# Kernel tuning notes

Measured on AMD Instinct MI355X. Metric: run time of the kernel, lower is better.

## Reference

```python
import jax, jax.numpy as jnp
import numpy as np

B, N, C, H = 8, 4096, 512, 8
HD = C // H  # head_dim = 64
SCALE = HD ** -0.5


def setup_inputs() -> dict:
    key = jax.random.key(0)
    k1, k2, k3, k4 = jax.random.split(key, 4)
    x1 = jax.random.normal(k1, (B, N, C), dtype=jnp.float32)
    x2 = jax.random.normal(k2, (B, N, C), dtype=jnp.float32)
    # nn.Linear(dim, 2*dim, bias=False) weights; stored as [in, out] for x @ W
    lim = 1.0 / np.sqrt(C)
    W_kv1 = jax.random.uniform(k3, (C, 2 * C), dtype=jnp.float32, minval=-lim, maxval=lim)
    W_kv2 = jax.random.uniform(k4, (C, 2 * C), dtype=jnp.float32, minval=-lim, maxval=lim)
    return {"x1": x1, "x2": x2, "W_kv1": W_kv1, "W_kv2": W_kv2}


def _heads(t):
    # [B, N, C] -> [B, H, N, HD]
    return t.reshape(B, N, H, HD).transpose(0, 2, 1, 3)


def _kv(x, W):
    kv = (x @ W).reshape(B, N, 2, H, HD)  # [B, N, 2, H, HD]
    kv = kv.transpose(2, 0, 3, 1, 4)      # [2, B, H, N, HD]
    return kv[0], kv[1]


def _ctx(k, v):
    # K^T V: [B, H, HD, HD], scaled then softmax over axis -2 (the k-feature axis)
    ctx = jnp.einsum("bhnd,bhne->bhde", k, v) * SCALE
    return jax.nn.softmax(ctx, axis=-2)


def reference(x1, x2, W_kv1, W_kv2):
    q1 = _heads(x1)
    q2 = _heads(x2)
    k1, v1 = _kv(x1, W_kv1)
    k2, v2 = _kv(x2, W_kv2)
    ctx1 = _ctx(k1, v1)
    ctx2 = _ctx(k2, v2)
    # cross: q1 attends via ctx2, q2 via ctx1
    o1 = jnp.einsum("bhnd,bhde->bhne", q1, ctx2).transpose(0, 2, 1, 3).reshape(B, N, C)
    o2 = jnp.einsum("bhnd,bhde->bhne", q2, ctx1).transpose(0, 2, 1, 3).reshape(B, N, C)
    return o1, o2
```

## Files before the change

### kernel.cpp

```cpp
#include <hip/hip_runtime.h>
#include <stdint.h>
#include <stddef.h>

#define NB 8
#define NSEQ 4096
#define NC 512
#define NH 8
#define SWZ(c) ((((c) >> 2) ^ (c)) & 7)

typedef __attribute__((ext_vector_type(4))) float f4;
typedef __attribute__((ext_vector_type(8))) short bf8;
typedef __attribute__((ext_vector_type(4))) short bf4;
typedef __attribute__((ext_vector_type(2))) unsigned int u32x2;
typedef __attribute__((ext_vector_type(4))) unsigned int u32x4;

__device__ __forceinline__ short f2bf(float f) {
  union { float f; unsigned int u; } v; v.f = f;
  unsigned int u = v.u + 0x7FFFu + ((v.u >> 16) & 1u);
  return (short)(u >> 16);
}
__device__ __forceinline__ float bf2f(short h) {
  union { unsigned int u; float f; } v;
  v.u = ((unsigned int)(unsigned short)h) << 16;
  return v.f;
}
__device__ __forceinline__ unsigned int cvtpk(float a, float b) {
  unsigned int r;
  asm("v_cvt_pk_bf16_f32 %0, %1, %2" : "=v"(r) : "v"(a), "v"(b));
  return r;
}

__global__ __launch_bounds__(256) void k_wt(const float* __restrict__ W0,
                                            const float* __restrict__ W1,
                                            short* __restrict__ Wth,
                                            short* __restrict__ Wtl) {
  __shared__ float t[64 * 65];
  int bid = blockIdx.x;
  int ot = bid & 15;
  int ct = (bid >> 4) & 7;
  int s = bid >> 7;
  const float* W = s ? W1 : W0;
  const float* src = W + (size_t)(ct * 64) * 1024 + ot * 64;
  int tid = threadIdx.x;
  int rr = tid >> 4, c4 = (tid & 15) * 4;
#pragma unroll
  for (int p = 0; p < 4; ++p) {
    int c = p * 16 + rr;
    f4 v = *(const f4*)&src[(size_t)c * 1024 + c4];
#pragma unroll
    for (int i = 0; i < 4; ++i) t[(c4 + i) * 65 + c] = v[i];
  }
  __syncthreads();
  size_t obase = (size_t)s * 524288 + (size_t)(ot * 64) * 512 + ct * 64;
#pragma unroll
  for (int p = 0; p < 4; ++p) {
    int o = p * 16 + rr;
    bf4 vh, vl;
#pragma unroll
    for (int i = 0; i < 4; ++i) {
      float v = t[o * 65 + c4 + i];
      short h = f2bf(v);
      vh[i] = h; vl[i] = f2bf(v - bf2f(h));
    }
    *(bf4*)&Wth[obase + (size_t)o * 512 + c4] = vh;
    *(bf4*)&Wtl[obase + (size_t)o * 512 + c4] = vl;
  }
}

__global__ __launch_bounds__(256, 3) void k_gram(const float* __restrict__ x0,
                                                 const float* __restrict__ x1,
                                                 float* __restrict__ G32a,
                                                 float* __restrict__ G32b) {
  __shared__ short bfA[64 * 128];
  __shared__ short bfB[64 * 128];
  int bid = blockIdx.x;
  int xcd = bid & 7;
  int j = bid >> 3;
  int kh = j >= 72;
  int jj = j - kh * 72;
  int sb = xcd + ((jj >= 36) ? 8 : 0);
  int p = (jj >= 36) ? (jj - 36) : jj;
  int ti = 0;
  while (p >= 8 - ti) { p -= 8 - ti; ++ti; }
  int tj = ti + p;
  int diag = (ti == tj);
  int s = sb >> 3, b = sb & 7;
  const float* x = s ? x1 : x0;
  const float* Axp = x + (size_t)b * NSEQ * NC + (size_t)kh * 2048 * NC + ti * 64;
  const float* Bxp = x + (size_t)b * NSEQ * NC + (size_t)kh * 2048 * NC + tj * 64;
  int tid = threadIdx.x;
  int lane = tid & 63;
  int w = tid >> 6;
  int c4 = (tid & 15) * 4;
  int n4 = (tid >> 4) * 4;
  int wr = w & 1, wc = w >> 1;
  int mrow = lane & 15;
  int kreg = lane >> 4;
  f4 z = {0.f, 0.f, 0.f, 0.f};
  f4 acc[2][2];
#pragma unroll
  for (int i = 0; i < 2; ++i)
#pragma unroll
    for (int jq = 0; jq < 2; ++jq) acc[i][jq] = z;

  f4 va[8], vb[8];
  auto load = [&](int k0) {
#pragma unroll
    for (int gq = 0; gq < 2; ++gq)
#pragma unroll
      for (int i = 0; i < 4; ++i)
        va[gq * 4 + i] = *(const f4*)&Axp[(size_t)(k0 + gq * 64 + n4 + i) * NC + c4];
    if (!diag) {
#pragma unroll
      for (int gq = 0; gq < 2; ++gq)
#pragma unroll
        for (int i = 0; i < 4; ++i)
          vb[gq * 4 + i] = *(const f4*)&Bxp[(size_t)(k0 + gq * 64 + n4 + i) * NC + c4];
    }
  };
  auto store = [&]() {
#pragma unroll
    for (int gq = 0; gq < 2; ++gq)
#pragma unroll
      for (int ci = 0; ci < 4; ++ci) {
        int c = c4 + ci;
        int slot = gq * 8 + (((n4 >> 3) ^ SWZ(c)) & 7);
        int soff = c * 128 + slot * 8 + (n4 & 7);
        u32x2 wa;
        wa[0] = cvtpk(va[gq * 4 + 0][ci], va[gq * 4 + 1][ci]);
        wa[1] = cvtpk(va[gq * 4 + 2][ci], va[gq * 4 + 3][ci]);
        *(u32x2*)&bfA[soff] = wa;
        if (!diag) {
          u32x2 wb;
          wb[0] = cvtpk(vb[gq * 4 + 0][ci], vb[gq * 4 + 1][ci]);
          wb[1] = cvtpk(vb[gq * 4 + 2][ci], vb[gq * 4 + 3][ci]);
          *(u32x2*)&bfB[soff] = wb;
        }
      }
  };
  auto comp = [&]() {
    const short* Bbuf = diag ? bfA : bfB;
#pragma unroll
    for (int kk = 0; kk < 4; ++kk) {
      int gr = kk * 4 + kreg;
      bf8 a[2], bb[2];
#pragma unroll
      for (int i = 0; i < 2; ++i) {
        int ra = wr * 32 + i * 16 + mrow;
        int sa = (gr & 8) | ((gr ^ SWZ(ra)) & 7);
        a[i] = *(const bf8*)&bfA[ra * 128 + sa * 8];
        int rb2 = wc * 32 + i * 16 + mrow;
        int sb2 = (gr & 8) | ((gr ^ SWZ(rb2)) & 7);
        bb[i] = *(const bf8*)&Bbuf[rb2 * 128 + sb2 * 8];
      }
#pragma unroll
      for (int i = 0; i < 2; ++i)
#pragma unroll
        for (int jq = 0; jq < 2; ++jq)
          acc[i][jq] = __builtin_amdgcn_mfma_f32_16x16x32_bf16(a[i], bb[jq], acc[i][jq], 0, 0, 0);
    }
  };

  load(0);
  for (int it = 0; it < 16; ++it) {
    store();
    __syncthreads();
    if (it < 15) load((it + 1) * 128);
    __builtin_amdgcn_sched_barrier(0);
    comp();
    __syncthreads();
  }

  float* Gp = (kh ? G32b : G32a) + (size_t)sb * NC * NC;
  int rb = ti * 64 + wr * 32 + (lane >> 4) * 4;
  int cb = tj * 64 + wc * 32 + (lane & 15);
#pragma unroll
  for (int i = 0; i < 2; ++i)
#pragma unroll
    for (int jq = 0; jq < 2; ++jq)
#pragma unroll
      for (int r = 0; r < 4; ++r)
        Gp[(size_t)(rb + i * 16 + r) * NC + cb + jq * 16] = acc[i][jq][r];
}

__global__ __launch_bounds__(256) void k_sym(const float* __restrict__ G32a,
                                             const float* __restrict__ G32b,
                                             short* __restrict__ Gh,
                                             short* __restrict__ Gl) {
  __shared__ float t[64 * 65];
  int bid = blockIdx.x;
  int tile = bid & 63;
  int sb = bid >> 6;
  int ti = tile >> 3, tj = tile & 7;
  int tr = ti > tj;
  size_t soff = (size_t)sb * 262144
              + (tr ? ((size_t)(tj * 64) * 512 + ti * 64)
                    : ((size_t)(ti * 64) * 512 + tj * 64));
  const float* srcA = G32a + soff;
  const float* srcB = G32b + soff;
  int tid = threadIdx.x;
  int rr = tid >> 4;
  int c4 = (tid & 15) * 4;
#pragma unroll
  for (int p = 0; p < 4; ++p) {
    int r = p * 16 + rr;
    f4 v = *(const f4*)&srcA[(size_t)r * 512 + c4];
    f4 v2 = *(const f4*)&srcB[(size_t)r * 512 + c4];
    v += v2;
    if (tr) {
#pragma unroll
      for (int i = 0; i < 4; ++i) t[(c4 + i) * 65 + r] = v[i];
    } else {
#pragma unroll
      for (int i = 0; i < 4; ++i) t[r * 65 + c4 + i] = v[i];
    }
  }
  __syncthreads();
  size_t obase = (size_t)sb * 262144 + (size_t)(ti * 64) * 512 + tj * 64;
#pragma unroll
  for (int p = 0; p < 4; ++p) {
    int r = p * 16 + rr;
    bf4 vh, vl;
#pragma unroll
    for (int i = 0; i < 4; ++i) {
      float v = t[r * 65 + c4 + i] * 0.125f;
      short h = f2bf(v);
      vh[i] = h; vl[i] = f2bf(v - bf2f(h));
    }
    *(bf4*)&Gh[obase + (size_t)r * 512 + c4] = vh;
    *(bf4*)&Gl[obase + (size_t)r * 512 + c4] = vl;
  }
}

__global__ __launch_bounds__(256) void k_t(const short* __restrict__ Wth,
                                           const short* __restrict__ Wtl,
                                           const short* __restrict__ Gh,
                                           const short* __restrict__ Gl,
                                           float* __restrict__ Ttf) {
  __shared__ short Ah[128 * 40];
  __shared__ short Al[128 * 40];
  __shared__ short Bh[128 * 40];
  __shared__ short Bl[128 * 40];
  int tid = threadIdx.x;
  int et = blockIdx.x & 3;
  int ct = blockIdx.x >> 2;
  int sb = blockIdx.y;
  int s = sb >> 3;
  const short* Avh = Wth + ((size_t)s * 1024 + 512 + (size_t)et * 128) * NC;
  const short* Avl = Wtl + ((size_t)s * 1024 + 512 + (size_t)et * 128) * NC;
  const short* Gph = Gh + (size_t)sb * 262144 + (size_t)(ct * 128) * 512;
  const short* Gpl = Gl + (size_t)sb * 262144 + (size_t)(ct * 128) * 512;
  int cc = tid >> 1;
  int kh = (tid & 1) * 16;
  int lane = tid & 63;
  int w = tid >> 6;
  int wm = (w & 1) * 64;
  int wn = (w >> 1) * 64;
  int mrow = lane & 15;
  int kcol = (lane >> 4) * 8;
  f4 z = {0.f, 0.f, 0.f, 0.f};
  f4 acc[4][4];
#pragma unroll
  for (int i = 0; i < 4; ++i)
#pragma unroll
    for (int j = 0; j < 4; ++j) acc[i][j] = z;

  for (int it = 0; it < 16; ++it) {
    int k0 = it * 32;
    __syncthreads();
    *(bf8*)&Ah[cc * 40 + kh]     = *(const bf8*)&Avh[(size_t)cc * NC + k0 + kh];
    *(bf8*)&Ah[cc * 40 + kh + 8] = *(const bf8*)&Avh[(size_t)cc * NC + k0 + kh + 8];
    *(bf8*)&Al[cc * 40 + kh]     = *(const bf8*)&Avl[(size_t)cc * NC + k0 + kh];
    *(bf8*)&Al[cc * 40 + kh + 8] = *(const bf8*)&Avl[(size_t)cc * NC + k0 + kh + 8];
    *(bf8*)&Bh[cc * 40 + kh]     = *(const bf8*)&Gph[(size_t)cc * 512 + k0 + kh];
    *(bf8*)&Bh[cc * 40 + kh + 8] = *(const bf8*)&Gph[(size_t)cc * 512 + k0 + kh + 8];
    *(bf8*)&Bl[cc * 40 + kh]     = *(const bf8*)&Gpl[(size_t)cc * 512 + k0 + kh];
    *(bf8*)&Bl[cc * 40 + kh + 8] = *(const bf8*)&Gpl[(size_t)cc * 512 + k0 + kh + 8];
    __syncthreads();
    bf8 ah[4], al[4], bh[4], bl[4];
#pragma unroll
    for (int i = 0; i < 4; ++i) {
      ah[i] = *(const bf8*)&Ah[(wm + i * 16 + mrow) * 40 + kcol];
      al[i] = *(const bf8*)&Al[(wm + i * 16 + mrow) * 40 + kcol];
      bh[i] = *(const bf8*)&Bh[(wn + i * 16 + mrow) * 40 + kcol];
      bl[i] = *(const bf8*)&Bl[(wn + i * 16 + mrow) * 40 + kcol];
    }
#pragma unroll
    for (int i = 0; i < 4; ++i)
#pragma unroll
      for (int j = 0; j < 4; ++j) {
        acc[i][j] = __builtin_amdgcn_mfma_f32_16x16x32_bf16(ah[i], bh[j], acc[i][j], 0, 0, 0);
        acc[i][j] = __builtin_amdgcn_mfma_f32_16x16x32_bf16(ah[i], bl[j], acc[i][j], 0, 0, 0);
        acc[i][j] = __builtin_amdgcn_mfma_f32_16x16x32_bf16(al[i], bh[j], acc[i][j], 0, 0, 0);
      }
  }
  float* Tp = Ttf + (size_t)sb * NC * NC;
  int rb = et * 128 + wm + (lane >> 4) * 4;
  int cb = ct * 128 + wn + (lane & 15);
#pragma unroll
  for (int i = 0; i < 4; ++i)
#pragma unroll
    for (int j = 0; j < 4; ++j)
#pragma unroll
      for (int r = 0; r < 4; ++r)
        Tp[(size_t)(rb + i * 16 + r) * NC + cb + j * 16] = acc[i][j][r];
}

__global__ __launch_bounds__(256) void k_ctx(const short* __restrict__ Wth,
                                             const short* __restrict__ Wtl,
                                             const float* __restrict__ Ttf,
                                             short* __restrict__ ctxT) {
  __shared__ short Ah[64 * 72];
  __shared__ short Al[64 * 72];
  __shared__ short Bh[64 * 72];
  __shared__ short Bl[64 * 72];
  __shared__ float Sf[64 * 68];
  int tid = threadIdx.x;
  int h = blockIdx.x & 7;
  int sb = blockIdx.x >> 3;
  int s = sb >> 3;
  const short* Akh = Wth + ((size_t)s * 1024 + (size_t)h * 64) * NC;
  const short* Akl = Wtl + ((size_t)s * 1024 + (size_t)h * 64) * NC;
  const float* Bt = Ttf + ((size_t)sb * NC + (size_t)h * 64) * NC;
  int cs = tid >> 3;
  int kg = (tid & 7) * 8;
  int lane = tid & 63;
  int w = tid >> 6;
  int mrow = lane & 15;
  int kcol = (lane >> 4) * 8;
  f4 z = {0.f, 0.f, 0.f, 0.f};
  f4 acc[4];
#pragma unroll
  for (int j = 0; j < 4; ++j) acc[j] = z;

  for (int it = 0; it < 8; ++it) {
    int k0 = it * 64;
    __syncthreads();
#pragma unroll
    for (int r = 0; r < 2; ++r) {
      int d = cs + r * 32;
      *(bf8*)&Ah[d * 72 + kg] = *(const bf8*)&Akh[(size_t)d * NC + k0 + kg];
      *(bf8*)&Al[d * 72 + kg] = *(const bf8*)&Akl[(size_t)d * NC + k0 + kg];
      f4 g0 = *(const f4*)&Bt[(size_t)d * NC + k0 + kg];
      f4 g1 = *(const f4*)&Bt[(size_t)d * NC + k0 + kg + 4];
      bf8 vh, vl;
#pragma unroll
      for (int i = 0; i < 4; ++i) {
        short hh = f2bf(g0[i]);
        vh[i] = hh; vl[i] = f2bf(g0[i] - bf2f(hh));
        hh = f2bf(g1[i]);
        vh[i + 4] = hh; vl[i + 4] = f2bf(g1[i] - bf2f(hh));
      }
      *(bf8*)&Bh[d * 72 + kg] = vh;
      *(bf8*)&Bl[d * 72 + kg] = vl;
    }
    __syncthreads();
#pragma unroll
    for (int kk = 0; kk < 2; ++kk) {
      bf8 ah = *(const bf8*)&Ah[(w * 16 + mrow) * 72 + kk * 32 + kcol];
      bf8 al = *(const bf8*)&Al[(w * 16 + mrow) * 72 + kk * 32 + kcol];
#pragma unroll
      for (int j = 0; j < 4; ++j) {
        bf8 bh = *(const bf8*)&Bh[(j * 16 + mrow) * 72 + kk * 32 + kcol];
        bf8 bl = *(const bf8*)&Bl[(j * 16 + mrow) * 72 + kk * 32 + kcol];
        acc[j] = __builtin_amdgcn_mfma_f32_16x16x32_bf16(ah, bh, acc[j], 0, 0, 0);
        acc[j] = __builtin_amdgcn_mfma_f32_16x16x32_bf16(ah, bl, acc[j], 0, 0, 0);
        acc[j] = __builtin_amdgcn_mfma_f32_16x16x32_bf16(al, bh, acc[j], 0, 0, 0);
      }
    }
  }
  __syncthreads();
#pragma unroll
  for (int j = 0; j < 4; ++j)
#pragma unroll
    for (int r = 0; r < 4; ++r)
      Sf[(w * 16 + (lane >> 4) * 4 + r) * 68 + j * 16 + (lane & 15)] = acc[j][r];
  __syncthreads();
  if (tid < 64) {
    int e = tid;
    float mx = -1e30f;
    for (int d = 0; d < 64; ++d) mx = fmaxf(mx, Sf[d * 68 + e]);
    float sum = 0.f;
    for (int d = 0; d < 64; ++d) {
      float ev = __expf(Sf[d * 68 + e] - mx);
      sum += ev;
      Sf[d * 68 + e] = ev;
    }
    float rs = 1.f / sum;
    short* cp = ctxT + (((size_t)sb * NH + h) * 64 + e) * 64;
    for (int d0 = 0; d0 < 64; d0 += 4) {
      bf4 ov;
      ov[0] = f2bf(Sf[(d0 + 0) * 68 + e] * rs);
      ov[1] = f2bf(Sf[(d0 + 1) * 68 + e] * rs);
      ov[2] = f2bf(Sf[(d0 + 2) * 68 + e] * rs);
      ov[3] = f2bf(Sf[(d0 + 3) * 68 + e] * rs);
      *(bf4*)&cp[d0] = ov;
    }
  }
}

__global__ __launch_bounds__(256) void k_o(const float* __restrict__ x0,
                                           const float* __restrict__ x1,
                                           const short* __restrict__ ctxT,
                                           float* __restrict__ out) {
  __shared__ short Ab[128 * 72];
  __shared__ short Bb[64 * 72];
  int tid = threadIdx.x;
  int bx = blockIdx.x;
  int nt = bx & 31;
  int h = (bx >> 5) & 7;
  int b = (bx >> 8) & 7;
  int so = bx >> 11;
  const float* x = so ? x1 : x0;
  const short* cp = ctxT + (((size_t)(1 - so) * NB + b) * NH + h) * 64 * 64;
  {
    int e = tid >> 2;
    int dg = (tid & 3) * 16;
    *(bf8*)&Bb[e * 72 + dg] = *(const bf8*)&cp[e * 64 + dg];
    *(bf8*)&Bb[e * 72 + dg + 8] = *(const bf8*)&cp[e * 64 + dg + 8];
  }
  const float* xp = x + ((size_t)b * NSEQ + (size_t)nt * 128) * NC + h * 64;
  {
    int n = tid >> 1;
    int dh = (tid & 1) * 32;
    const float* row = xp + (size_t)n * NC + dh;
#pragma unroll
    for (int q = 0; q < 4; ++q) {
      f4 v0 = *(const f4*)&row[q * 8];
      f4 v1 = *(const f4*)&row[q * 8 + 4];
      u32x4 pw;
      pw[0] = cvtpk(v0[0], v0[1]);
      pw[1] = cvtpk(v0[2], v0[3]);
      pw[2] = cvtpk(v1[0], v1[1]);
      pw[3] = cvtpk(v1[2], v1[3]);
      *(u32x4*)&Ab[n * 72 + dh + q * 8] = pw;
    }
  }
  __syncthreads();
  int lane = tid & 63;
  int w = tid >> 6;
  int mrow = lane & 15;
  int kcol = (lane >> 4) * 8;
  f4 z = {0.f, 0.f, 0.f, 0.f};
  f4 acc[2][4];
#pragma unroll
  for (int i = 0; i < 2; ++i)
#pragma unroll
    for (int j = 0; j < 4; ++j) acc[i][j] = z;
#pragma unroll
  for (int kk = 0; kk < 2; ++kk) {
    bf8 a0 = *(const bf8*)&Ab[(w * 32 + mrow) * 72 + kk * 32 + kcol];
    bf8 a1 = *(const bf8*)&Ab[(w * 32 + 16 + mrow) * 72 + kk * 32 + kcol];
#pragma unroll
    for (int j = 0; j < 4; ++j) {
      bf8 bv = *(const bf8*)&Bb[(j * 16 + mrow) * 72 + kk * 32 + kcol];
      acc[0][j] = __builtin_amdgcn_mfma_f32_16x16x32_bf16(a0, bv, acc[0][j], 0, 0, 0);
      acc[1][j] = __builtin_amdgcn_mfma_f32_16x16x32_bf16(a1, bv, acc[1][j], 0, 0, 0);
    }
  }
  float* op = out + (size_t)so * ((size_t)NB * NSEQ * NC)
            + ((size_t)b * NSEQ + (size_t)nt * 128) * NC + h * 64;
#pragma unroll
  for (int i = 0; i < 2; ++i)
#pragma unroll
    for (int j = 0; j < 4; ++j)
#pragma unroll
      for (int r = 0; r < 4; ++r)
        op[(size_t)(w * 32 + i * 16 + (lane >> 4) * 4 + r) * NC + j * 16 + (lane & 15)] = acc[i][j][r];
}

extern "C" void kernel_launch(void* const* d_in, const int* in_sizes, int n_in,
                              void* d_out, int out_size, void* d_ws, size_t ws_size,
                              hipStream_t stream) {
  const float* x1 = (const float*)d_in[0];
  const float* x2 = (const float*)d_in[1];
  const float* W1 = (const float*)d_in[2];
  const float* W2 = (const float*)d_in[3];
  float* out = (float*)d_out;
  char* ws = (char*)d_ws;
  float* Ttf  = (float*)ws;
  short* Gh   = (short*)(ws + 16777216);
  short* Gl   = (short*)(ws + 25165824);
  float* G32a = (float*)(ws + 33554432);
  float* G32b = (float*)(ws + 50331648);
  short* Wth  = (short*)(ws + 67108864);
  short* Wtl  = (short*)(ws + 69206016);
  short* ctxT = (short*)(ws + 71303168);

  hipLaunchKernelGGL(k_wt,   dim3(256),    dim3(256), 0, stream, W1, W2, Wth, Wtl);
  hipLaunchKernelGGL(k_gram, dim3(1152),   dim3(256), 0, stream, x1, x2, G32a, G32b);
  hipLaunchKernelGGL(k_sym,  dim3(1024),   dim3(256), 0, stream, G32a, G32b, Gh, Gl);
  hipLaunchKernelGGL(k_t,    dim3(16, 16), dim3(256), 0, stream, Wth, Wtl, Gh, Gl, Ttf);
  hipLaunchKernelGGL(k_ctx,  dim3(128),    dim3(256), 0, stream, Wth, Wtl, Ttf, ctxT);
  hipLaunchKernelGGL(k_o,    dim3(4096),   dim3(256), 0, stream, x1, x2, ctxT, out);
}
```

Baseline: 168.4 us.

## Split Gram reduction four ways and stage k_o output through LDS

The Gram kernel now splits the sequence dimension into four partial sums instead of two, doubling the grid to 2304 blocks. Each block runs half as many k-iterations, and k_sym sums four partial buffers. This gives more parallelism and better occupancy in the Gram phase, at the cost of extra fp32 partial traffic and reduction reads. Separately, k_o now writes its accumulators to a padded LDS tile and then stores coalesced float4 rows, which should improve global write efficiency. The workspace layout is reshuffled so the partial buffers alias the T buffer region.

```diff
diff --git a/kernel.cpp b/kernel.cpp
--- a/kernel.cpp
+++ b/kernel.cpp
@@ -69,25 +69,24 @@
 
 __global__ __launch_bounds__(256, 3) void k_gram(const float* __restrict__ x0,
                                                  const float* __restrict__ x1,
-                                                 float* __restrict__ G32a,
-                                                 float* __restrict__ G32b) {
+                                                 float* __restrict__ G32p) {
   __shared__ short bfA[64 * 128];
   __shared__ short bfB[64 * 128];
   int bid = blockIdx.x;
   int xcd = bid & 7;
-  int j = bid >> 3;
-  int kh = j >= 72;
-  int jj = j - kh * 72;
-  int sb = xcd + ((jj >= 36) ? 8 : 0);
-  int p = (jj >= 36) ? (jj - 36) : jj;
+  int iL = bid >> 3;
+  int g = iL / 36;
+  int p = iL - g * 36;
+  int kq = g & 3;
+  int sb = xcd + (g >> 2) * 8;
   int ti = 0;
   while (p >= 8 - ti) { p -= 8 - ti; ++ti; }
   int tj = ti + p;
   int diag = (ti == tj);
   int s = sb >> 3, b = sb & 7;
   const float* x = s ? x1 : x0;
-  const float* Axp = x + (size_t)b * NSEQ * NC + (size_t)kh * 2048 * NC + ti * 64;
-  const float* Bxp = x + (size_t)b * NSEQ * NC + (size_t)kh * 2048 * NC + tj * 64;
+  const float* Axp = x + (size_t)b * NSEQ * NC + (size_t)kq * 1024 * NC + ti * 64;
+  const float* Bxp = x + (size_t)b * NSEQ * NC + (size_t)kq * 1024 * NC + tj * 64;
   int tid = threadIdx.x;
   int lane = tid & 63;
   int w = tid >> 6;
@@ -162,16 +161,16 @@
   };
 
   load(0);
-  for (int it = 0; it < 16; ++it) {
+  for (int it = 0; it < 8; ++it) {
     store();
     __syncthreads();
-    if (it < 15) load((it + 1) * 128);
+    if (it < 7) load((it + 1) * 128);
     __builtin_amdgcn_sched_barrier(0);
     comp();
     __syncthreads();
   }
 
-  float* Gp = (kh ? G32b : G32a) + (size_t)sb * NC * NC;
+  float* Gp = G32p + (size_t)kq * 4194304 + (size_t)sb * NC * NC;
   int rb = ti * 64 + wr * 32 + (lane >> 4) * 4;
   int cb = tj * 64 + wc * 32 + (lane & 15);
 #pragma unroll
@@ -183,8 +182,7 @@
         Gp[(size_t)(rb + i * 16 + r) * NC + cb + jq * 16] = acc[i][jq][r];
 }
 
-__global__ __launch_bounds__(256) void k_sym(const float* __restrict__ G32a,
-                                             const float* __restrict__ G32b,
+__global__ __launch_bounds__(256) void k_sym(const float* __restrict__ G32p,
                                              short* __restrict__ Gh,
                                              short* __restrict__ Gl) {
   __shared__ float t[64 * 65];
@@ -196,17 +194,18 @@
   size_t soff = (size_t)sb * 262144
               + (tr ? ((size_t)(tj * 64) * 512 + ti * 64)
                     : ((size_t)(ti * 64) * 512 + tj * 64));
-  const float* srcA = G32a + soff;
-  const float* srcB = G32b + soff;
   int tid = threadIdx.x;
   int rr = tid >> 4;
   int c4 = (tid & 15) * 4;
 #pragma unroll
   for (int p = 0; p < 4; ++p) {
     int r = p * 16 + rr;
-    f4 v = *(const f4*)&srcA[(size_t)r * 512 + c4];
-    f4 v2 = *(const f4*)&srcB[(size_t)r * 512 + c4];
-    v += v2;
+    size_t o = soff + (size_t)r * 512 + c4;
+    f4 v = *(const f4*)&G32p[o];
+    f4 v1 = *(const f4*)&G32p[o + 4194304];
+    f4 v2 = *(const f4*)&G32p[o + 2 * 4194304];
+    f4 v3 = *(const f4*)&G32p[o + 3 * 4194304];
+    v = (v + v1) + (v2 + v3);
     if (tr) {
 #pragma unroll
       for (int i = 0; i < 4; ++i) t[(c4 + i) * 65 + r] = v[i];
@@ -403,8 +402,10 @@
                                            const float* __restrict__ x1,
                                            const short* __restrict__ ctxT,
                                            float* __restrict__ out) {
-  __shared__ short Ab[128 * 72];
-  __shared__ short Bb[64 * 72];
+  __shared__ float U[8704];
+  short* Ab = (short*)U;
+  short* Bb = (short*)U + 128 * 72;
+  float* OutT = U;
   int tid = threadIdx.x;
   int bx = blockIdx.x;
   int nt = bx & 31;
@@ -458,15 +459,22 @@
       acc[1][j] = __builtin_amdgcn_mfma_f32_16x16x32_bf16(a1, bv, acc[1][j], 0, 0, 0);
     }
   }
-  float* op = out + (size_t)so * ((size_t)NB * NSEQ * NC)
-            + ((size_t)b * NSEQ + (size_t)nt * 128) * NC + h * 64;
+  __syncthreads();
 #pragma unroll
   for (int i = 0; i < 2; ++i)
 #pragma unroll
     for (int j = 0; j < 4; ++j)
 #pragma unroll
       for (int r = 0; r < 4; ++r)
-        op[(size_t)(w * 32 + i * 16 + (lane >> 4) * 4 + r) * NC + j * 16 + (lane & 15)] = acc[i][j][r];
+        OutT[(w * 32 + i * 16 + (lane >> 4) * 4 + r) * 68 + j * 16 + (lane & 15)] = acc[i][j][r];
+  __syncthreads();
+  int r2 = tid >> 1;
+  int ch = (tid & 1) * 32;
+  float* op2 = out + (size_t)so * ((size_t)NB * NSEQ * NC)
+             + ((size_t)b * NSEQ + (size_t)nt * 128 + r2) * NC + h * 64 + ch;
+#pragma unroll
+  for (int q = 0; q < 8; ++q)
+    *(f4*)&op2[q * 4] = *(const f4*)&OutT[r2 * 68 + ch + q * 4];
 }
 
 extern "C" void kernel_launch(void* const* d_in, const int* in_sizes, int n_in,
@@ -478,18 +486,17 @@
   const float* W2 = (const float*)d_in[3];
   float* out = (float*)d_out;
   char* ws = (char*)d_ws;
+  float* G32p = (float*)ws;
   float* Ttf  = (float*)ws;
-  short* Gh   = (short*)(ws + 16777216);
-  short* Gl   = (short*)(ws + 25165824);
-  float* G32a = (float*)(ws + 33554432);
-  float* G32b = (float*)(ws + 50331648);
   short* Wth  = (short*)(ws + 67108864);
   short* Wtl  = (short*)(ws + 69206016);
   short* ctxT = (short*)(ws + 71303168);
+  short* Gh   = (short*)(ws + 72351744);
+  short* Gl   = (short*)(ws + 80740352);
 
   hipLaunchKernelGGL(k_wt,   dim3(256),    dim3(256), 0, stream, W1, W2, Wth, Wtl);
-  hipLaunchKernelGGL(k_gram, dim3(1152),   dim3(256), 0, stream, x1, x2, G32a, G32b);
-  hipLaunchKernelGGL(k_sym,  dim3(1024),   dim3(256), 0, stream, G32a, G32b, Gh, Gl);
+  hipLaunchKernelGGL(k_gram, dim3(2304),   dim3(256), 0, stream, x1, x2, G32p);
+  hipLaunchKernelGGL(k_sym,  dim3(1024),   dim3(256), 0, stream, G32p, Gh, Gl);
   hipLaunchKernelGGL(k_t,    dim3(16, 16), dim3(256), 0, stream, Wth, Wtl, Gh, Gl, Ttf);
   hipLaunchKernelGGL(k_ctx,  dim3(128),    dim3(256), 0, stream, Wth, Wtl, Ttf, ctxT);
   hipLaunchKernelGGL(k_o,    dim3(4096),   dim3(256), 0, stream, x1, x2, ctxT, out);
```

Measured after the change: 176.6 us. 1.05x slower.
